# Kernel tuning notes

Measured on AMD Instinct MI355X. Metric: run time of the kernel, lower is better.

## Reference

```python
import jax, jax.numpy as jnp
import numpy as np

HSIG_SCALE = 0.16666667  # matches MyHSigmoid's * 0.16666667

def setup_inputs() -> dict:
    key = jax.random.key(0)
    k = jax.random.split(key, 5)
    B, C, H, W, MID = 32, 256, 56, 56, 64
    return {
        "x": jax.random.normal(k[0], (B, C, H, W), dtype=jnp.float32),
        "w1": jax.random.normal(k[1], (MID, C), dtype=jnp.float32) * 0.05,
        "b1": jax.random.normal(k[2], (MID,), dtype=jnp.float32) * 0.05,
        "w2": jax.random.normal(k[3], (C, MID), dtype=jnp.float32) * 0.05,
        "b2": jax.random.normal(k[4], (C,), dtype=jnp.float32) * 0.05,
        "inject": 0, "current_epoch": 0, "counter": 0, "inject_index": 0,
    }

def reference(x, w1, b1, w2, b2, inject, current_epoch, counter, inject_index):
    # global average pool over H,W -> [B, C]
    pooled = jnp.mean(x, axis=(2, 3))
    # 1x1 conv reduce (GEMV) + ReLU
    h = jax.nn.relu(jnp.einsum('bc,mc->bm', pooled, w1) + b1)
    # 1x1 conv expand + hard-sigmoid (relu6(y+3) * 0.16666667)
    y = jnp.einsum('bm,cm->bc', h, w2) + b2
    gate = jnp.clip(y + 3.0, 0.0, 6.0) * HSIG_SCALE
    # broadcast channel gate over spatial dims
    return x * gate[:, :, None, None]
```

## Files before the change

### kernel.cpp

```cpp
#include <hip/hip_runtime.h>
#include <stdint.h>

#define BATCH 32
#define CH    256
#define MID   64
#define HW    3136
#define HWV   784

typedef __attribute__((ext_vector_type(4))) float fvec4;

__global__ __launch_bounds__(256) void se_pool_h(const fvec4* __restrict__ x,
                                                 const float* __restrict__ w1,
                                                 float* __restrict__ hpre) {
    const int p = blockIdx.x;
    const int b = p >> 8;
    const int c = p & 255;
    const int t = threadIdx.x;

    const fvec4* base = x + (size_t)p * HWV;
    float sum = 0.0f;
    for (int i = t; i < HWV; i += 256) {
        fvec4 v = base[i];
        sum += v.x + v.y + v.z + v.w;
    }
    #pragma unroll
    for (int off = 32; off > 0; off >>= 1) sum += __shfl_down(sum, off, 64);

    __shared__ float part[4];
    if ((t & 63) == 0) part[t >> 6] = sum;
    __syncthreads();

    if (t < MID) {
        const float pv =
            (part[0] + part[1] + part[2] + part[3]) * (1.0f / (float)HW);
        atomicAdd(&hpre[b * MID + t], pv * w1[t * CH + c]);
    }
}

__global__ __launch_bounds__(256) void se_scale(const fvec4* __restrict__ x,
                                                const float* __restrict__ hpre,
                                                const float* __restrict__ b1,
                                                const float* __restrict__ w2,
                                                const float* __restrict__ b2,
                                                fvec4* __restrict__ out) {
    const int p = blockIdx.x;
    const int b = p >> 8;
    const int c = p & 255;
    const int t = threadIdx.x;

    const fvec4* xb = x + (size_t)p * HWV;
    fvec4 v0 = xb[t];
    fvec4 v1 = xb[t + 256];
    fvec4 v2 = xb[t + 512];
    fvec4 v3 = {0.f, 0.f, 0.f, 0.f};
    if (t < 16) v3 = xb[t + 768];

    __shared__ float gsh;
    if (t < MID) {
        float hv = fmaxf(hpre[b * MID + t] + b1[t], 0.0f);
        float yv = hv * w2[c * MID + t];
        #pragma unroll
        for (int off = 32; off > 0; off >>= 1) yv += __shfl_down(yv, off, 64);
        if (t == 0) {
            gsh = fminf(fmaxf(yv + b2[c] + 3.0f, 0.0f), 6.0f) * 0.16666667f;
        }
    }
    __syncthreads();
    const float g = gsh;

    fvec4* ob = out + (size_t)p * HWV;
    __builtin_nontemporal_store(v0 * g, ob + t);
    __builtin_nontemporal_store(v1 * g, ob + t + 256);
    __builtin_nontemporal_store(v2 * g, ob + t + 512);
    if (t < 16) __builtin_nontemporal_store(v3 * g, ob + t + 768);
}

extern "C" void kernel_launch(void* const* d_in, const int* in_sizes, int n_in,
                              void* d_out, int out_size, void* d_ws, size_t ws_size,
                              hipStream_t stream) {
    (void)in_sizes; (void)n_in; (void)out_size; (void)ws_size;

    const float* x  = (const float*)d_in[0];
    const float* w1 = (const float*)d_in[1];
    const float* b1 = (const float*)d_in[2];
    const float* w2 = (const float*)d_in[3];
    const float* b2 = (const float*)d_in[4];

    float* hpre = (float*)d_ws;

    hipMemsetAsync(hpre, 0, BATCH * MID * sizeof(float), stream);
    se_pool_h<<<BATCH * CH, 256, 0, stream>>>((const fvec4*)x, w1, hpre);
    se_scale<<<BATCH * CH, 256, 0, stream>>>((const fvec4*)x, hpre,
                                             b1, w2, b2, (fvec4*)d_out);
}
```

Baseline: 211.9 us.

## Split SE into pool, MLP and scale kernels, dropping atomics and memset

The pooling kernel now assigns one wavefront per (batch, channel) plane and writes the pooled means directly. This removes the per-block atomicAdd of 64 partial products and the memset that went before it. A new small kernel computes the two-layer MLP and hard-sigmoid gate once per batch. The scale kernel then reads a precomputed gate instead of redoing the w2 dot product in every block. The cost is an extra kernel launch and a serial dependency through a 32-block kernel, in exchange for less atomic traffic and less redundant gate arithmetic.

```diff
diff --git a/kernel.cpp b/kernel.cpp
--- a/kernel.cpp
+++ b/kernel.cpp
@@ -6,69 +6,79 @@
 #define MID   64
 #define HW    3136
 #define HWV   784
+#define NPLANES (BATCH * CH)
 
 typedef __attribute__((ext_vector_type(4))) float fvec4;
 
-__global__ __launch_bounds__(256) void se_pool_h(const fvec4* __restrict__ x,
-                                                 const float* __restrict__ w1,
-                                                 float* __restrict__ hpre) {
-    const int p = blockIdx.x;
-    const int b = p >> 8;
-    const int c = p & 255;
+__global__ __launch_bounds__(256) void se_pool(const fvec4* __restrict__ x,
+                                               float* __restrict__ pooled) {
+    const int gw   = (blockIdx.x << 2) + (threadIdx.x >> 6);
+    const int lane = threadIdx.x & 63;
+
+    const fvec4* base = x + (size_t)gw * HWV;
+    float s = 0.0f;
+    #pragma unroll 4
+    for (int i = lane; i < HWV; i += 64) {
+        fvec4 v = base[i];
+        s += (v.x + v.y) + (v.z + v.w);
+    }
+    #pragma unroll
+    for (int off = 32; off > 0; off >>= 1) s += __shfl_down(s, off, 64);
+    if (lane == 0) pooled[gw] = s * (1.0f / (float)HW);
+}
+
+__global__ __launch_bounds__(256) void se_mlp(float* __restrict__ buf,
+                                              const float* __restrict__ w1,
+                                              const float* __restrict__ b1,
+                                              const float* __restrict__ w2,
+                                              const float* __restrict__ b2) {
+    const int b = blockIdx.x;
     const int t = threadIdx.x;
 
-    const fvec4* base = x + (size_t)p * HWV;
-    float sum = 0.0f;
-    for (int i = t; i < HWV; i += 256) {
-        fvec4 v = base[i];
-        sum += v.x + v.y + v.z + v.w;
-    }
-    #pragma unroll
-    for (int off = 32; off > 0; off >>= 1) sum += __shfl_down(sum, off, 64);
+    __shared__ float pl[CH];
+    __shared__ float hq[4][MID];
+    __shared__ float hsh[MID];
 
-    __shared__ float part[4];
-    if ((t & 63) == 0) part[t >> 6] = sum;
+    pl[t] = buf[b * CH + t];
+    __syncthreads();
+
+    const int m = t & 63, q = t >> 6;
+    const float* w1r = w1 + m * CH + q * 64;
+    const float* plq = pl + q * 64;
+    float acc = 0.0f;
+    #pragma unroll 8
+    for (int c = 0; c < 64; ++c) acc += plq[c] * w1r[c];
+    hq[q][m] = acc;
     __syncthreads();
 
     if (t < MID) {
-        const float pv =
-            (part[0] + part[1] + part[2] + part[3]) * (1.0f / (float)HW);
-        atomicAdd(&hpre[b * MID + t], pv * w1[t * CH + c]);
+        hsh[t] = fmaxf(hq[0][t] + hq[1][t] + hq[2][t] + hq[3][t] + b1[t], 0.0f);
     }
+    __syncthreads();
+
+    const float* w2r = w2 + t * MID;
+    float y = b2[t];
+    #pragma unroll 8
+    for (int mm = 0; mm < MID; ++mm) y += hsh[mm] * w2r[mm];
+    buf[b * CH + t] = fminf(fmaxf(y + 3.0f, 0.0f), 6.0f) * 0.16666667f;
 }
 
 __global__ __launch_bounds__(256) void se_scale(const fvec4* __restrict__ x,
-                                                const float* __restrict__ hpre,
-                                                const float* __restrict__ b1,
-                                                const float* __restrict__ w2,
-                                                const float* __restrict__ b2,
+                                                const float* __restrict__ gate,
                                                 fvec4* __restrict__ out) {
     const int p = blockIdx.x;
-    const int b = p >> 8;
-    const int c = p & 255;
     const int t = threadIdx.x;
+    const float g = gate[p];
 
     const fvec4* xb = x + (size_t)p * HWV;
+    fvec4* ob = out + (size_t)p * HWV;
+
     fvec4 v0 = xb[t];
     fvec4 v1 = xb[t + 256];
     fvec4 v2 = xb[t + 512];
     fvec4 v3 = {0.f, 0.f, 0.f, 0.f};
     if (t < 16) v3 = xb[t + 768];
 
-    __shared__ float gsh;
-    if (t < MID) {
-        float hv = fmaxf(hpre[b * MID + t] + b1[t], 0.0f);
-        float yv = hv * w2[c * MID + t];
-        #pragma unroll
-        for (int off = 32; off > 0; off >>= 1) yv += __shfl_down(yv, off, 64);
-        if (t == 0) {
-            gsh = fminf(fmaxf(yv + b2[c] + 3.0f, 0.0f), 6.0f) * 0.16666667f;
-        }
-    }
-    __syncthreads();
-    const float g = gsh;
-
-    fvec4* ob = out + (size_t)p * HWV;
     __builtin_nontemporal_store(v0 * g, ob + t);
     __builtin_nontemporal_store(v1 * g, ob + t + 256);
     __builtin_nontemporal_store(v2 * g, ob + t + 512);
@@ -86,10 +96,9 @@
     const float* w2 = (const float*)d_in[3];
     const float* b2 = (const float*)d_in[4];
 
-    float* hpre = (float*)d_ws;
+    float* buf = (float*)d_ws;
 
-    hipMemsetAsync(hpre, 0, BATCH * MID * sizeof(float), stream);
-    se_pool_h<<<BATCH * CH, 256, 0, stream>>>((const fvec4*)x, w1, hpre);
-    se_scale<<<BATCH * CH, 256, 0, stream>>>((const fvec4*)x, hpre,
-                                             b1, w2, b2, (fvec4*)d_out);
+    se_pool<<<NPLANES / 4, 256, 0, stream>>>((const fvec4*)x, buf);
+    se_mlp<<<BATCH, 256, 0, stream>>>(buf, w1, b1, w2, b2);
+    se_scale<<<NPLANES, 256, 0, stream>>>((const fvec4*)x, buf, (fvec4*)d_out);
 }
```

New measurement: 214.2 us. Within noise of the previous version (+1.1%).
